# Kernel optimization log

Hardware: AMD Instinct MI355X
Metric: run time of the kernel (lower is better)

## Reference

```python
import jax, jax.numpy as jnp
import numpy as np

D_MODEL = 1024
N_HEAD = 16


def setup_inputs() -> dict:
    key = jax.random.key(0)
    ks = jax.random.split(key, 7)
    B, L, D = 2, 2048, D_MODEL
    s = 0.02
    return {
        "x": jax.random.normal(ks[0], (B, L, D), dtype=jnp.float32),
        "W_kq": jax.random.normal(ks[1], (D, 2 * D), dtype=jnp.float32) * s,
        "b_kq": jax.random.normal(ks[2], (2 * D,), dtype=jnp.float32) * s,
        "W_v": jax.random.normal(ks[3], (D, D), dtype=jnp.float32) * s,
        "b_v": jax.random.normal(ks[4], (D,), dtype=jnp.float32) * s,
        "W_o": jax.random.normal(ks[5], (D, D), dtype=jnp.float32) * s,
        "b_o": jax.random.normal(ks[6], (D,), dtype=jnp.float32) * s,
    }


def reference(x, W_kq, b_kq, W_v, b_v, W_o, b_o):
    B, L, D = x.shape
    H = N_HEAD
    dh = D // H
    kq = x @ W_kq + b_kq            # (B, L, 2D); split order: k first, then q
    k = kq[..., :D].reshape(B, L, H, dh)
    q = kq[..., D:].reshape(B, L, H, dh)
    v = (x @ W_v + b_v).reshape(B, L, H, dh)
    scale = 1.0 / jnp.sqrt(jnp.float32(dh))
    scores = jnp.einsum('blhd,bmhd->bhlm', q, k) * scale  # (B, H, L, L)
    causal = jnp.tril(jnp.ones((L, L), dtype=bool))
    scores = jnp.where(causal, scores, -jnp.inf)
    attn = jax.nn.softmax(scores, axis=-1)
    out = jnp.einsum('bhlm,bmhd->blhd', attn, v).reshape(B, L, D)
    out = out @ W_o + b_o
    return jnp.squeeze(out)
```

## Files before the change

kernel.cpp:

```cpp
#include <hip/hip_runtime.h>
#include <cstdint>


#define LSEQ 2048
#define DM   1024
#define BL   4096

using frag_ab = __attribute__((ext_vector_type(8))) short;
using half8   = __attribute__((ext_vector_type(8))) _Float16;
using half4   = __attribute__((ext_vector_type(4))) _Float16;
using f32x4   = __attribute__((ext_vector_type(4))) float;

__device__ __forceinline__ unsigned short f2bf(float f) {
  unsigned int u = __float_as_uint(f);
  u += 0x7fffu + ((u >> 16) & 1u);
  return (unsigned short)(u >> 16);
}

__device__ __forceinline__ void load_lds16(const void* g, void* l) {
  __builtin_amdgcn_global_load_lds(
      (const __attribute__((address_space(1))) unsigned int*)g,
      (__attribute__((address_space(3))) unsigned int*)l, 16, 0, 0);
}


__global__ __launch_bounds__(256) void prep_kernel(
    const float* __restrict__ x, unsigned short* __restrict__ xb,
    const float* __restrict__ W_kq, const float* __restrict__ W_v,
    const float* __restrict__ W_o,
    unsigned short* __restrict__ wcat, _Float16* __restrict__ wot)
{
  const int bid = blockIdx.x;
  const int tid = threadIdx.x;

  if (bid < 4096) {
    const int i = bid * 256 + tid;
    const float4 v = *(const float4*)&x[(size_t)i * 4];
    ushort4 o;
    o.x = f2bf(v.x); o.y = f2bf(v.y); o.z = f2bf(v.z); o.w = f2bf(v.w);
    *(ushort4*)&xb[(size_t)i * 4] = o;
    return;
  }

  __shared__ float tile[32][33];
  const int r  = tid >> 3;
  const int c4 = (tid & 7) * 4;

  const float* W;
  int N, nb, kb, which;
  if (bid < 6144) {
    const int b2 = bid - 4096;
    W = W_kq; N = 2048; nb = (b2 & 63) * 32; kb = (b2 >> 6) * 32; which = 0;
  } else if (bid < 7168) {
    const int b2 = bid - 6144;
    W = W_v;  N = 1024; nb = (b2 & 31) * 32; kb = (b2 >> 5) * 32; which = 1;
  } else {
    const int b2 = bid - 7168;
    W = W_o;  N = 1024; nb = (b2 & 31) * 32; kb = (b2 >> 5) * 32; which = 2;
  }

  const float4 v = *(const float4*)&W[(size_t)(kb + r) * N + nb + c4];
  tile[r][c4 + 0] = v.x; tile[r][c4 + 1] = v.y;
  tile[r][c4 + 2] = v.z; tile[r][c4 + 3] = v.w;
  __syncthreads();

  if (which == 2) {
    half4 o;
    o[0] = (_Float16)tile[c4 + 0][r];
    o[1] = (_Float16)tile[c4 + 1][r];
    o[2] = (_Float16)tile[c4 + 2][r];
    o[3] = (_Float16)tile[c4 + 3][r];
    *(half4*)&wot[(size_t)(nb + r) * 1024 + kb + c4] = o;
  } else {
    ushort4 o;
    o.x = f2bf(tile[c4 + 0][r]);
    o.y = f2bf(tile[c4 + 1][r]);
    o.z = f2bf(tile[c4 + 2][r]);
    o.w = f2bf(tile[c4 + 3][r]);
    unsigned short* dst = (which == 0) ? wcat : wcat + 2097152;
    *(ushort4*)&dst[(size_t)(nb + r) * 1024 + kb + c4] = o;
  }
}


__global__ __launch_bounds__(256) void gemm_kqv(
    const unsigned short* __restrict__ A, const unsigned short* __restrict__ Bt,
    const float* __restrict__ b_kq, const float* __restrict__ b_v,
    unsigned short* __restrict__ kqb, _Float16* __restrict__ vtb)
{
  const int tid  = threadIdx.x;
  const int lane = tid & 63;
  const int w    = tid >> 6;
  const int wm   = (w >> 1) * 64;
  const int wn   = (w & 1) * 64;
  const int n0   = blockIdx.x * 128;
  const int m0   = blockIdx.y * 128;
  const int quad = lane >> 4;
  const int l15  = lane & 15;
  const int K    = 1024;

  __shared__ __align__(16) unsigned short As[128 * 64];
  __shared__ __align__(16) unsigned short Bs[128 * 64];

  const int srow = lane >> 3;
  const int sc   = (lane & 7) ^ srow;

  const unsigned short* gA = A  + (size_t)(m0 + w * 32 + srow) * K + sc * 8;
  const unsigned short* gB = Bt + (size_t)(n0 + w * 32 + srow) * K + sc * 8;

  f32x4 acc[4][4] = {};

  for (int k0 = 0; k0 < K; k0 += 64) {
    __syncthreads();
#pragma unroll
    for (int i = 0; i < 4; ++i) {
      load_lds16(gA + (size_t)i * 8 * K + k0, &As[(w * 32 + i * 8) * 64 + lane * 8]);
      load_lds16(gB + (size_t)i * 8 * K + k0, &Bs[(w * 32 + i * 8) * 64 + lane * 8]);
    }
    __syncthreads();
#pragma unroll
    for (int kf = 0; kf < 2; ++kf) {
      frag_ab af[4], bf[4];
#pragma unroll
      for (int t = 0; t < 4; ++t) {
        const int ra = wm + t * 16 + l15;
        const int pa = (kf * 4 + quad) ^ (ra & 7);
        af[t] = *(const frag_ab*)&As[ra * 64 + pa * 8];
        const int rb = wn + t * 16 + l15;
        const int pb = (kf * 4 + quad) ^ (rb & 7);
        bf[t] = *(const frag_ab*)&Bs[rb * 64 + pb * 8];
      }
#pragma unroll
      for (int i = 0; i < 4; ++i)
#pragma unroll
        for (int j = 0; j < 4; ++j)
          acc[i][j] = __builtin_amdgcn_mfma_f32_16x16x32_bf16(
              af[i], bf[j], acc[i][j], 0, 0, 0);
    }
  }

  if (n0 >= 2048) {
#pragma unroll
    for (int i = 0; i < 4; ++i)
#pragma unroll
      for (int j = 0; j < 4; ++j) {
        const int row0 = m0 + wm + i * 16 + quad * 4;
        const int col  = n0 - 2048 + wn + j * 16 + l15;
        const float bv = b_v[col];
        half4 pk;
        pk[0] = (_Float16)(acc[i][j][0] + bv);
        pk[1] = (_Float16)(acc[i][j][1] + bv);
        pk[2] = (_Float16)(acc[i][j][2] + bv);
        pk[3] = (_Float16)(acc[i][j][3] + bv);
        *(half4*)&vtb[(size_t)col * BL + row0] = pk;
      }
  } else {
    const float sc2 = (n0 + wn >= 1024) ? 0.125f : 1.0f;
#pragma unroll
    for (int i = 0; i < 4; ++i)
#pragma unroll
      for (int j = 0; j < 4; ++j) {
        const int row0 = m0 + wm + i * 16 + quad * 4;
        const int col  = n0 + wn + j * 16 + l15;
        const float bv = b_kq[col];
#pragma unroll
        for (int r = 0; r < 4; ++r)
          kqb[(size_t)(row0 + r) * 2048 + col] = f2bf((acc[i][j][r] + bv) * sc2);
      }
  }
}


__global__ __launch_bounds__(256, 4) void gemm_out(
    const _Float16* __restrict__ A, const _Float16* __restrict__ Bt,
    const float* __restrict__ bias, float* __restrict__ C)
{
  const int tid  = threadIdx.x;
  const int lane = tid & 63;
  const int w    = tid >> 6;
  const int wm   = (w >> 1) * 64;
  const int wn   = (w & 1) * 32;
  const int n0   = blockIdx.x * 64;
  const int m0   = blockIdx.y * 128;
  const int quad = lane >> 4;
  const int l15  = lane & 15;
  const int K    = 1024;

  __shared__ __align__(16) _Float16 As[128 * 64];
  __shared__ __align__(16) _Float16 Bs[64 * 64];

  const int srow = lane >> 3;
  const int sc   = (lane & 7) ^ srow;

  const _Float16* gA = A  + (size_t)(m0 + w * 32 + srow) * K + sc * 8;
  const _Float16* gB = Bt + (size_t)(n0 + w * 16 + srow) * K + sc * 8;

  f32x4 acc[4][2] = {};

  for (int k0 = 0; k0 < K; k0 += 64) {
    __syncthreads();
#pragma unroll
    for (int i = 0; i < 4; ++i)
      load_lds16(gA + (size_t)i * 8 * K + k0, &As[(w * 32 + i * 8) * 64 + lane * 8]);
#pragma unroll
    for (int i = 0; i < 2; ++i)
      load_lds16(gB + (size_t)i * 8 * K + k0, &Bs[(w * 16 + i * 8) * 64 + lane * 8]);
    __syncthreads();
#pragma unroll
    for (int kf = 0; kf < 2; ++kf) {
      half8 af[4], bf[2];
#pragma unroll
      for (int t = 0; t < 4; ++t) {
        const int ra = wm + t * 16 + l15;
        const int pa = (kf * 4 + quad) ^ (ra & 7);
        af[t] = *(const half8*)&As[ra * 64 + pa * 8];
      }
#pragma unroll
      for (int t = 0; t < 2; ++t) {
        const int rb = wn + t * 16 + l15;
        const int pb = (kf * 4 + quad) ^ (rb & 7);
        bf[t] = *(const half8*)&Bs[rb * 64 + pb * 8];
      }
#pragma unroll
      for (int i = 0; i < 4; ++i)
#pragma unroll
        for (int j = 0; j < 2; ++j)
          acc[i][j] = __builtin_amdgcn_mfma_f32_16x16x32_f16(
              af[i], bf[j], acc[i][j], 0, 0, 0);
    }
  }

#pragma unroll
  for (int i = 0; i < 4; ++i)
#pragma unroll
    for (int j = 0; j < 2; ++j) {
      const int row0 = m0 + wm + i * 16 + quad * 4;
      const int col  = n0 + wn + j * 16 + l15;
      const float bv = bias[col];
#pragma unroll
      for (int r = 0; r < 4; ++r)
        C[(size_t)(row0 + r) * DM + col] = acc[i][j][r] + bv;
    }
}


__global__ __launch_bounds__(256) void attn_mfma(
    const unsigned short* __restrict__ kq, const _Float16* __restrict__ vt,
    _Float16* __restrict__ att)
{
  const int tid  = threadIdx.x;
  const int lane = tid & 63;
  const int w    = tid >> 6;
  const int bx   = blockIdx.x;
  const int qt   = 31 - (bx >> 5);
  const int bh   = bx & 31;
  const int b    = bh >> 4;
  const int h    = bh & 15;
  const int q0   = qt * 64;
  const int quad = lane >> 4;
  const int l15  = lane & 15;

  __shared__ __align__(16) unsigned short Ks[128 * 64];
  __shared__ __align__(16) _Float16      Vs[64 * 128];

#pragma unroll
  for (int i = 0; i < 2; ++i) {
    const int L = i * 256 + tid;
    const int row = L >> 3, c = L & 7;
    const unsigned short* g = kq + (size_t)(b * LSEQ + q0 + row) * 2048
                                 + DM + h * 64 + ((c ^ (row & 7)) * 8);
    load_lds16(g, &Ks[(size_t)L * 8]);
  }
  __syncthreads();
  frag_ab qa[2];
#pragma unroll
  for (int kf = 0; kf < 2; ++kf) {
    const int row = w * 16 + l15;
    const int c = (kf * 4 + quad) ^ (row & 7);
    qa[kf] = *(const frag_ab*)&Ks[row * 64 + c * 8];
  }

  f32x4 oacc[4] = {};
  float mrow = -3e38f, lrow = 0.f;
  const int nk = (qt + 2) >> 1;

  for (int kt = 0; kt < nk; ++kt) {
    const int k0 = kt * 128;
    __syncthreads();
#pragma unroll
    for (int i = 0; i < 4; ++i) {
      const int L = i * 256 + tid;
      {
        const int row = L >> 3, c = L & 7;
        const unsigned short* g = kq + (size_t)(b * LSEQ + k0 + row) * 2048
                                     + h * 64 + ((c ^ (row & 7)) * 8);
        load_lds16(g, &Ks[(size_t)L * 8]);
      }
      {
        const int row = L >> 4, c16 = L & 15;
        const _Float16* g = vt + (size_t)(h * 64 + row) * BL
                               + b * LSEQ + k0 + ((c16 ^ (row & 15)) * 8);
        load_lds16(g, &Vs[(size_t)L * 8]);
      }
    }
    __syncthreads();

    f32x4 st[8];
#pragma unroll
    for (int mt = 0; mt < 8; ++mt) {
      f32x4 s = {};
#pragma unroll
      for (int kf = 0; kf < 2; ++kf) {
        const int row = mt * 16 + l15;
        const int c = (kf * 4 + quad) ^ (row & 7);
        const frag_ab kfrag = *(const frag_ab*)&Ks[row * 64 + c * 8];
        s = __builtin_amdgcn_mfma_f32_16x16x32_bf16(kfrag, qa[kf], s, 0, 0, 0);
      }
      st[mt] = s;
    }

    if (kt == nk - 1) {
      const int qg = q0 + w * 16 + l15;
#pragma unroll
      for (int mt = 0; mt < 8; ++mt)
#pragma unroll
        for (int r = 0; r < 4; ++r)
          if (k0 + mt * 16 + quad * 4 + r > qg) st[mt][r] = -3e38f;
    }

    float mx = -3e38f;
#pragma unroll
    for (int mt = 0; mt < 8; ++mt)
#pragma unroll
      for (int r = 0; r < 4; ++r) mx = fmaxf(mx, st[mt][r]);
    mx = fmaxf(mx, __shfl_xor(mx, 16));
    mx = fmaxf(mx, __shfl_xor(mx, 32));
    const float mnew  = fmaxf(mrow, mx);
    const float alpha = __expf(mrow - mnew);
    half4 pf[8];
    float rsum = 0.f;
#pragma unroll
    for (int mt = 0; mt < 8; ++mt)
#pragma unroll
      for (int r = 0; r < 4; ++r) {
        const float e = __expf(st[mt][r] - mnew);
        rsum += e;
        pf[mt][r] = (_Float16)e;
      }
    rsum += __shfl_xor(rsum, 16);
    rsum += __shfl_xor(rsum, 32);
    lrow = lrow * alpha + rsum;
    mrow = mnew;

    float aq[4];
#pragma unroll
    for (int r = 0; r < 4; ++r) aq[r] = __shfl(alpha, quad * 4 + r);
#pragma unroll
    for (int dt = 0; dt < 4; ++dt)
#pragma unroll
      for (int r = 0; r < 4; ++r) oacc[dt][r] *= aq[r];

#pragma unroll
    for (int c8 = 0; c8 < 8; ++c8) {
#pragma unroll
      for (int dt = 0; dt < 4; ++dt) {
        const int g16 = 2 * c8 + (quad >> 1);
        const half4 vf = *(const half4*)&Vs[(dt * 16 + l15) * 128
                                            + ((g16 ^ l15) << 3) + ((quad & 1) << 2)];
        oacc[dt] = __builtin_amdgcn_mfma_f32_16x16x16f16(pf[c8], vf, oacc[dt], 0, 0, 0);
      }
    }
  }

  float lq[4];
#pragma unroll
  for (int r = 0; r < 4; ++r) lq[r] = 1.0f / __shfl(lrow, quad * 4 + r);
#pragma unroll
  for (int dt = 0; dt < 4; ++dt)
#pragma unroll
    for (int r = 0; r < 4; ++r) {
      const int row = b * LSEQ + q0 + w * 16 + quad * 4 + r;
      const int col = h * 64 + dt * 16 + l15;
      att[(size_t)row * DM + col] = (_Float16)(oacc[dt][r] * lq[r]);
    }
}


extern "C" void kernel_launch(void* const* d_in, const int* in_sizes, int n_in,
                              void* d_out, int out_size, void* d_ws, size_t ws_size,
                              hipStream_t stream)
{
  const float* x    = (const float*)d_in[0];
  const float* W_kq = (const float*)d_in[1];
  const float* b_kq = (const float*)d_in[2];
  const float* W_v  = (const float*)d_in[3];
  const float* b_v  = (const float*)d_in[4];
  const float* W_o  = (const float*)d_in[5];
  const float* b_o  = (const float*)d_in[6];

  unsigned short* ws   = (unsigned short*)d_ws;
  unsigned short* xb   = ws;
  unsigned short* wcat = xb   + 4194304;
  _Float16*       wot  = (_Float16*)(wcat + 3145728);
  unsigned short* kqb  = (unsigned short*)(wot + 1048576);
  _Float16*       vtb  = (_Float16*)(kqb + 8388608);
  _Float16*       attb = vtb + 4194304;

  prep_kernel<<<8192, 256, 0, stream>>>(x, xb, W_kq, W_v, W_o, wcat, wot);
  gemm_kqv<<<dim3(24, 32), 256, 0, stream>>>(xb, wcat, b_kq, b_v, kqb, vtb);
  attn_mfma<<<1024, 256, 0, stream>>>(kqb, vtb, attb);
  gemm_out<<<dim3(16, 32), 256, 0, stream>>>(attb, wot, b_o, (float*)d_out);
}
```

Baseline: 188.0 us.

## Pair light and heavy causal query tiles per block to share K/V loads

Each attention block now handles two query tiles, pr and 31-pr, so every block does the same total causal work. K/V tiles loaded into LDS are reused by both tiles while the shorter one is still active. The grid is halved to 512 blocks. The cost is twice the accumulator and register state per thread, which may lower occupancy, and fewer blocks on the device.

After: 200.4 us. +6.6%, slower.

```diff
diff --git a/kernel.cpp b/kernel.cpp
--- a/kernel.cpp
+++ b/kernel.cpp
@@ -244,6 +244,77 @@
 }
 
 
+__device__ __forceinline__ void attn_step(
+    const unsigned short* Ks, const _Float16* Vs, const frag_ab* qa,
+    int k0, int qg, bool last, int quad, int l15,
+    float& mrow, float& lrow, f32x4* oacc)
+{
+  f32x4 st[8];
+#pragma unroll
+  for (int mt = 0; mt < 8; ++mt) {
+    f32x4 s = {};
+#pragma unroll
+    for (int kf = 0; kf < 2; ++kf) {
+      const int row = mt * 16 + l15;
+      const int c = (kf * 4 + quad) ^ (row & 7);
+      const frag_ab kfrag = *(const frag_ab*)&Ks[row * 64 + c * 8];
+      s = __builtin_amdgcn_mfma_f32_16x16x32_bf16(kfrag, qa[kf], s, 0, 0, 0);
+    }
+    st[mt] = s;
+  }
+
+  if (last) {
+#pragma unroll
+    for (int mt = 0; mt < 8; ++mt)
+#pragma unroll
+      for (int r = 0; r < 4; ++r)
+        if (k0 + mt * 16 + quad * 4 + r > qg) st[mt][r] = -3e38f;
+  }
+
+  float mx = -3e38f;
+#pragma unroll
+  for (int mt = 0; mt < 8; ++mt)
+#pragma unroll
+    for (int r = 0; r < 4; ++r) mx = fmaxf(mx, st[mt][r]);
+  mx = fmaxf(mx, __shfl_xor(mx, 16));
+  mx = fmaxf(mx, __shfl_xor(mx, 32));
+  const float mnew  = fmaxf(mrow, mx);
+  const float alpha = __expf(mrow - mnew);
+  half4 pf[8];
+  float rsum = 0.f;
+#pragma unroll
+  for (int mt = 0; mt < 8; ++mt)
+#pragma unroll
+    for (int r = 0; r < 4; ++r) {
+      const float e = __expf(st[mt][r] - mnew);
+      rsum += e;
+      pf[mt][r] = (_Float16)e;
+    }
+  rsum += __shfl_xor(rsum, 16);
+  rsum += __shfl_xor(rsum, 32);
+  lrow = lrow * alpha + rsum;
+  mrow = mnew;
+
+  float aq[4];
+#pragma unroll
+  for (int r = 0; r < 4; ++r) aq[r] = __shfl(alpha, quad * 4 + r);
+#pragma unroll
+  for (int dt = 0; dt < 4; ++dt)
+#pragma unroll
+    for (int r = 0; r < 4; ++r) oacc[dt][r] *= aq[r];
+
+#pragma unroll
+  for (int c8 = 0; c8 < 8; ++c8) {
+#pragma unroll
+    for (int dt = 0; dt < 4; ++dt) {
+      const int g16 = 2 * c8 + (quad >> 1);
+      const half4 vf = *(const half4*)&Vs[(dt * 16 + l15) * 128
+                                          + ((g16 ^ l15) << 3) + ((quad & 1) << 2)];
+      oacc[dt] = __builtin_amdgcn_mfma_f32_16x16x16f16(pf[c8], vf, oacc[dt], 0, 0, 0);
+    }
+  }
+}
+
 __global__ __launch_bounds__(256) void attn_mfma(
     const unsigned short* __restrict__ kq, const _Float16* __restrict__ vt,
     _Float16* __restrict__ att)
@@ -252,39 +323,51 @@
   const int lane = tid & 63;
   const int w    = tid >> 6;
   const int bx   = blockIdx.x;
-  const int qt   = 31 - (bx >> 5);
+  const int pr   = bx >> 5;
   const int bh   = bx & 31;
   const int b    = bh >> 4;
   const int h    = bh & 15;
-  const int q0   = qt * 64;
+  const int tA   = pr;
+  const int tB   = 31 - pr;
+  const int qA0  = tA * 64;
+  const int qB0  = tB * 64;
+  const int nkA  = (tA + 2) >> 1;
+  const int nkB  = (tB + 2) >> 1;
   const int quad = lane >> 4;
   const int l15  = lane & 15;
 
   __shared__ __align__(16) unsigned short Ks[128 * 64];
   __shared__ __align__(16) _Float16      Vs[64 * 128];
 
-#pragma unroll
-  for (int i = 0; i < 2; ++i) {
-    const int L = i * 256 + tid;
-    const int row = L >> 3, c = L & 7;
-    const unsigned short* g = kq + (size_t)(b * LSEQ + q0 + row) * 2048
-                                 + DM + h * 64 + ((c ^ (row & 7)) * 8);
-    load_lds16(g, &Ks[(size_t)L * 8]);
-  }
-  __syncthreads();
-  frag_ab qa[2];
-#pragma unroll
-  for (int kf = 0; kf < 2; ++kf) {
-    const int row = w * 16 + l15;
-    const int c = (kf * 4 + quad) ^ (row & 7);
-    qa[kf] = *(const frag_ab*)&Ks[row * 64 + c * 8];
-  }
-
-  f32x4 oacc[4] = {};
-  float mrow = -3e38f, lrow = 0.f;
-  const int nk = (qt + 2) >> 1;
-
-  for (int kt = 0; kt < nk; ++kt) {
+  frag_ab qaA[2], qaB[2];
+#pragma unroll
+  for (int t = 0; t < 2; ++t) {
+    const int q0 = t ? qB0 : qA0;
+    if (t) __syncthreads();
+#pragma unroll
+    for (int i = 0; i < 2; ++i) {
+      const int L = i * 256 + tid;
+      const int row = L >> 3, c = L & 7;
+      const unsigned short* g = kq + (size_t)(b * LSEQ + q0 + row) * 2048
+                                   + DM + h * 64 + ((c ^ (row & 7)) * 8);
+      load_lds16(g, &Ks[(size_t)L * 8]);
+    }
+    __syncthreads();
+#pragma unroll
+    for (int kf = 0; kf < 2; ++kf) {
+      const int row = w * 16 + l15;
+      const int c = (kf * 4 + quad) ^ (row & 7);
+      const frag_ab f = *(const frag_ab*)&Ks[row * 64 + c * 8];
+      if (t) qaB[kf] = f; else qaA[kf] = f;
+    }
+  }
+
+  f32x4 oaccA[4] = {}, oaccB[4] = {};
+  float mA = -3e38f, lA = 0.f, mB = -3e38f, lB = 0.f;
+  const int qgA = qA0 + w * 16 + l15;
+  const int qgB = qB0 + w * 16 + l15;
+
+  for (int kt = 0; kt < nkB; ++kt) {
     const int k0 = kt * 128;
     __syncthreads();
 #pragma unroll
@@ -305,84 +388,28 @@
     }
     __syncthreads();
 
-    f32x4 st[8];
-#pragma unroll
-    for (int mt = 0; mt < 8; ++mt) {
-      f32x4 s = {};
-#pragma unroll
-      for (int kf = 0; kf < 2; ++kf) {
-        const int row = mt * 16 + l15;
-        const int c = (kf * 4 + quad) ^ (row & 7);
-        const frag_ab kfrag = *(const frag_ab*)&Ks[row * 64 + c * 8];
-        s = __builtin_amdgcn_mfma_f32_16x16x32_bf16(kfrag, qa[kf], s, 0, 0, 0);
-      }
-      st[mt] = s;
-    }
-
-    if (kt == nk - 1) {
-      const int qg = q0 + w * 16 + l15;
-#pragma unroll
-      for (int mt = 0; mt < 8; ++mt)
-#pragma unroll
-        for (int r = 0; r < 4; ++r)
-          if (k0 + mt * 16 + quad * 4 + r > qg) st[mt][r] = -3e38f;
-    }
-
-    float mx = -3e38f;
-#pragma unroll
-    for (int mt = 0; mt < 8; ++mt)
-#pragma unroll
-      for (int r = 0; r < 4; ++r) mx = fmaxf(mx, st[mt][r]);
-    mx = fmaxf(mx, __shfl_xor(mx, 16));
-    mx = fmaxf(mx, __shfl_xor(mx, 32));
-    const float mnew  = fmaxf(mrow, mx);
-    const float alpha = __expf(mrow - mnew);
-    half4 pf[8];
-    float rsum = 0.f;
-#pragma unroll
-    for (int mt = 0; mt < 8; ++mt)
+    attn_step(Ks, Vs, qaB, k0, qgB, kt == nkB - 1, quad, l15, mB, lB, oaccB);
+    if (kt < nkA)
+      attn_step(Ks, Vs, qaA, k0, qgA, kt == nkA - 1, quad, l15, mA, lA, oaccA);
+  }
+
+#pragma unroll
+  for (int t = 0; t < 2; ++t) {
+    const int q0 = t ? qB0 : qA0;
+    const float lrow = t ? lB : lA;
+    const f32x4* oacc = t ? oaccB : oaccA;
+    float lq[4];
+#pragma unroll
+    for (int r = 0; r < 4; ++r) lq[r] = 1.0f / __shfl(lrow, quad * 4 + r);
+#pragma unroll
+    for (int dt = 0; dt < 4; ++dt)
 #pragma unroll
       for (int r = 0; r < 4; ++r) {
-        const float e = __expf(st[mt][r] - mnew);
-        rsum += e;
-        pf[mt][r] = (_Float16)e;
-      }
-    rsum += __shfl_xor(rsum, 16);
-    rsum += __shfl_xor(rsum, 32);
-    lrow = lrow * alpha + rsum;
-    mrow = mnew;
-
-    float aq[4];
-#pragma unroll
-    for (int r = 0; r < 4; ++r) aq[r] = __shfl(alpha, quad * 4 + r);
-#pragma unroll
-    for (int dt = 0; dt < 4; ++dt)
-#pragma unroll
-      for (int r = 0; r < 4; ++r) oacc[dt][r] *= aq[r];
-
-#pragma unroll
-    for (int c8 = 0; c8 < 8; ++c8) {
-#pragma unroll
-      for (int dt = 0; dt < 4; ++dt) {
-        const int g16 = 2 * c8 + (quad >> 1);
-        const half4 vf = *(const half4*)&Vs[(dt * 16 + l15) * 128
-                                            + ((g16 ^ l15) << 3) + ((quad & 1) << 2)];
-        oacc[dt] = __builtin_amdgcn_mfma_f32_16x16x16f16(pf[c8], vf, oacc[dt], 0, 0, 0);
-      }
-    }
-  }
-
-  float lq[4];
-#pragma unroll
-  for (int r = 0; r < 4; ++r) lq[r] = 1.0f / __shfl(lrow, quad * 4 + r);
-#pragma unroll
-  for (int dt = 0; dt < 4; ++dt)
-#pragma unroll
-    for (int r = 0; r < 4; ++r) {
-      const int row = b * LSEQ + q0 + w * 16 + quad * 4 + r;
-      const int col = h * 64 + dt * 16 + l15;
-      att[(size_t)row * DM + col] = (_Float16)(oacc[dt][r] * lq[r]);
-    }
+        const int row = b * LSEQ + q0 + w * 16 + quad * 4 + r;
+        const int col = h * 64 + dt * 16 + l15;
+        att[(size_t)row * DM + col] = (_Float16)(oacc[dt][r] * lq[r]);
+      }
+  }
 }
 
 
@@ -408,6 +435,6 @@
 
   prep_kernel<<<8192, 256, 0, stream>>>(x, xb, W_kq, W_v, W_o, wcat, wot);
   gemm_kqv<<<dim3(24, 32), 256, 0, stream>>>(xb, wcat, b_kq, b_v, kqb, vtb);
-  attn_mfma<<<1024, 256, 0, stream>>>(kqb, vtb, attb);
+  attn_mfma<<<512, 256, 0, stream>>>(kqb, vtb, attb);
   gemm_out<<<dim3(16, 32), 256, 0, stream>>>(attb, wot, b_o, (float*)d_out);
 }
```
